# Kernel optimization log

Hardware: AMD Instinct MI355X
Metric: run time of the kernel (lower is better)

The kernel has to match this reference:

```python
import jax, jax.numpy as jnp
import numpy as np

B, H, S, DH = 2, 16, 2048, 64
MASK_FILL = -10000.0


def setup_inputs() -> dict:
    key = jax.random.key(0)
    kq, kk, kv = jax.random.split(key, 3)
    q = jax.random.normal(kq, (B, H, S, DH), dtype=jnp.float32)
    k = jax.random.normal(kk, (B, H, S, DH), dtype=jnp.float32)
    v = jax.random.normal(kv, (B, H, S, DH), dtype=jnp.float32)
    # causal mask: True where attention is disallowed (upper triangle)
    mask = jnp.triu(jnp.ones((S, S), dtype=jnp.bool_), k=1)
    return {"q": q, "k": k, "v": v, "mask": mask}


def reference(q, k, v, mask):
    scale = 1.0 / jnp.sqrt(jnp.asarray(k.shape[-1], dtype=q.dtype))
    # scores: [B, H, S_q, S_k]
    scores = jnp.einsum("bhqd,bhkd->bhqk", q, k) * scale
    # additive mask: masked_fill on a zeros [S_k, S_v] matrix -> -10000 where mask
    attn_bias = jnp.where(mask, jnp.asarray(MASK_FILL, dtype=k.dtype),
                          jnp.asarray(0.0, dtype=k.dtype))
    scores = scores + attn_bias  # broadcast over batch/heads
    attn = jax.nn.softmax(scores, axis=-1)
    # dropout_rate = 0.0 -> identity
    return jnp.einsum("bhqk,bhkd->bhqd", attn, v)
```

## Files before the change

kernel.cpp:

```cpp
#include <hip/hip_runtime.h>


#define S_LEN  2048
#define DHDIM  64
#define NHEADS 32
#define LDP    72
#define M2     23.083120654223414f
#define QSCALE 0.18033688011117658f

typedef __attribute__((ext_vector_type(8))) short bf16x8;
typedef __attribute__((ext_vector_type(4))) float f32x4;

__device__ __constant__ unsigned char T_QT[48] = {
    31,31,30,15, 30,29,29,28,14, 28,27,27,26,13, 26,25,25,24,12,
    24,23,23,22,11, 22,21,21,20,10, 20,19,19,18,9, 18,17,17,16,8,
    16,7, 6,5,4,3,2,1,0};
__device__ __constant__ unsigned char T_K0[48] = {
    0,16,0,0, 16,0,15,0,0, 15,0,14,0,0, 14,0,13,0,0,
    13,0,12,0,0, 12,0,11,0,0, 11,0,10,0,0, 10,0,9,0,0,
    9,0, 0,0,0,0,0,0,0};
__device__ __constant__ unsigned char T_K1[48] = {
    16,32,16,16, 31,15,30,15,15, 29,14,28,14,14, 27,13,26,13,13,
    25,12,24,12,12, 23,11,22,11,11, 21,10,20,10,10, 19,9,18,9,9,
    17,8, 7,6,5,4,3,2,1};

__device__ __forceinline__ float fast_exp2(float x) {
#if __has_builtin(__builtin_amdgcn_exp2f)
    return __builtin_amdgcn_exp2f(x);
#else
    return exp2f(x);
#endif
}
__device__ __forceinline__ unsigned short f2bf(float f) {
    unsigned u = __float_as_uint(f);
    return (unsigned short)((u + 0x7fffu + ((u >> 16) & 1u)) >> 16);
}
__device__ __forceinline__ void ld8(const float* p, float* f) {
    float4 a = *(const float4*)p, b = *(const float4*)(p + 4);
    f[0]=a.x; f[1]=a.y; f[2]=a.z; f[3]=a.w; f[4]=b.x; f[5]=b.y; f[6]=b.z; f[7]=b.w;
}
__device__ __forceinline__ uint4 pack8(const float* f, float scale) {
    union { uint4 v; unsigned short s[8]; } w;
    #pragma unroll
    for (int j = 0; j < 8; j++) w.s[j] = f2bf(f[j] * scale);
    return w.v;
}
__device__ __forceinline__ unsigned packhi(float a, float b) {
#if __has_builtin(__builtin_amdgcn_perm)
    return __builtin_amdgcn_perm(__float_as_uint(b), __float_as_uint(a), 0x07060302u);
#else
    return (__float_as_uint(a) >> 16) | (__float_as_uint(b) & 0xffff0000u);
#endif
}

__global__ __launch_bounds__(256) void prep(
    const float* __restrict__ Qf, const float* __restrict__ Kf,
    const float* __restrict__ Vf, unsigned short* __restrict__ qb,
    unsigned short* __restrict__ kb, unsigned short* __restrict__ vtb)
{
    const int st = blockIdx.x, bh = blockIdx.y;
    __shared__ unsigned lt32[64][LDP / 2];
    const float* vp = Vf + ((size_t)bh * S_LEN + st * 64) * DHDIM;
    {
        const int c = threadIdx.x;
        const int sp = c >> 3;
        const int d0 = (c & 7) * 8;
        float fa[8], fb[8];
        ld8(vp + (2 * sp) * DHDIM + d0, fa);
        ld8(vp + (2 * sp + 1) * DHDIM + d0, fb);
        #pragma unroll
        for (int j = 0; j < 8; j++) {
            int d = d0 + j;
            int colw = (sp & 3) | ((((sp >> 2) ^ (d >> 3)) & 7) << 2);
            lt32[d][colw] = (unsigned)f2bf(fa[j]) | ((unsigned)f2bf(fb[j]) << 16);
        }
    }
    size_t off = ((size_t)(bh * 32 + st) * 4096) + (size_t)threadIdx.x * 16;
    float f[8];
    ld8(Qf + off, f);     *(uint4*)(qb + off)     = pack8(f, QSCALE);
    ld8(Qf + off + 8, f); *(uint4*)(qb + off + 8) = pack8(f, QSCALE);
    ld8(Kf + off, f);     *(uint4*)(kb + off)     = pack8(f, 1.0f);
    ld8(Kf + off + 8, f); *(uint4*)(kb + off + 8) = pack8(f, 1.0f);
    __syncthreads();
    unsigned short* op = vtb + (size_t)bh * DHDIM * S_LEN + st * 64;
    for (int c = threadIdx.x; c < 512; c += 256) {
        int d = c >> 3, q = c & 7;
        int colw = ((q ^ (d >> 3)) & 7) << 2;
        *(uint4*)(op + (size_t)d * S_LEN + q * 8) = *(const uint4*)&lt32[d][colw & ~3 ? colw : colw];
    }
}

__global__ __launch_bounds__(256) void fattn_splitk(
    const unsigned short* __restrict__ Qp, const unsigned short* __restrict__ Kp,
    const unsigned short* __restrict__ Vp,
    float* __restrict__ pO, float* __restrict__ pL, float* __restrict__ O)
{
    __shared__ unsigned short smem[192 * LDP];
    unsigned short (*ks)[LDP]  = (unsigned short(*)[LDP])smem;
    unsigned short (*vts)[LDP] = (unsigned short(*)[LDP])(smem + 64 * LDP);
    unsigned short (*qs)[LDP]  = (unsigned short(*)[LDP])(smem + 128 * LDP);
    unsigned short (*pst)[LDP] = qs;

    const int bh   = blockIdx.x;
    const int rank = blockIdx.y;
    const int qt   = T_QT[rank];
    const int k0   = T_K0[rank];
    const int k1   = T_K1[rank];
    const bool whole = (k1 - k0 == qt + 1);

    const int tid = threadIdx.x;
    const int wave = tid >> 6, lane = tid & 63;
    const int quad = lane >> 4, l16 = lane & 15;

    {
        const unsigned short* src = Qp + ((size_t)bh * S_LEN + qt * 64) * DHDIM;
        for (int c = tid; c < 512; c += 256) {
            int row = c >> 3, c8 = (c & 7) * 8;
            *(uint4*)&qs[row][c8] = *(const uint4*)(src + row * DHDIM + c8);
        }
    }
    __syncthreads();

    const int prow = wave * 16 + l16;
    const bf16x8 bq0 = *(const bf16x8*)&qs[prow][quad * 8];
    const bf16x8 bq1 = *(const bf16x8*)&qs[prow][32 + quad * 8];

    bf16x8 ones;
    #pragma unroll
    for (int j = 0; j < 8; j++) ones[j] = (short)0x3F80;

    f32x4 of[4];
    f32x4 of_l = (f32x4){0.f, 0.f, 0.f, 0.f};
    #pragma unroll
    for (int n = 0; n < 4; n++) of[n] = (f32x4){0.f, 0.f, 0.f, 0.f};

    const unsigned short* Kbh = Kp + (size_t)bh * S_LEN * DHDIM;
    const unsigned short* Vbh = Vp + (size_t)bh * DHDIM * S_LEN;
    const int sr = tid >> 3, sc = (tid & 7) * 8;
    uint4 kr0, kr1, vr0, vr1;
    {
        const unsigned short* ksrc = Kbh + (size_t)k0 * 64 * DHDIM;
        const unsigned short* vsrc = Vbh + k0 * 64;
        kr0 = *(const uint4*)(ksrc + sr * DHDIM + sc);
        kr1 = *(const uint4*)(ksrc + (sr + 32) * DHDIM + sc);
        vr0 = *(const uint4*)(vsrc + (size_t)sr * S_LEN + sc);
        vr1 = *(const uint4*)(vsrc + (size_t)(sr + 32) * S_LEN + sc);
    }

    for (int kt = k0; kt < k1; kt++) {
        __syncthreads();

        *(uint4*)&ks[sr][sc]       = kr0;
        *(uint4*)&ks[sr + 32][sc]  = kr1;
        *(uint4*)&vts[sr][sc]      = vr0;
        *(uint4*)&vts[sr + 32][sc] = vr1;

        if (kt + 1 < k1) {
            const unsigned short* ksrc = Kbh + (size_t)(kt + 1) * 64 * DHDIM;
            const unsigned short* vsrc = Vbh + (kt + 1) * 64;
            kr0 = *(const uint4*)(ksrc + sr * DHDIM + sc);
            kr1 = *(const uint4*)(ksrc + (sr + 32) * DHDIM + sc);
            vr0 = *(const uint4*)(vsrc + (size_t)sr * S_LEN + sc);
            vr1 = *(const uint4*)(vsrc + (size_t)(sr + 32) * S_LEN + sc);
        }
        __syncthreads();

        f32x4 sf[4];
        #pragma unroll
        for (int n = 0; n < 4; n++) {
            bf16x8 ak0 = *(const bf16x8*)&ks[n * 16 + l16][quad * 8];
            bf16x8 ak1 = *(const bf16x8*)&ks[n * 16 + l16][32 + quad * 8];
            sf[n] = (f32x4){-M2, -M2, -M2, -M2};
            sf[n] = __builtin_amdgcn_mfma_f32_16x16x32_bf16(ak0, bq0, sf[n], 0, 0, 0);
            sf[n] = __builtin_amdgcn_mfma_f32_16x16x32_bf16(ak1, bq1, sf[n], 0, 0, 0);
        }

        const bool diag = (kt == qt);
        #pragma unroll
        for (int n = 0; n < 4; n++) {
            float p[4];
            #pragma unroll
            for (int r = 0; r < 4; r++) {
                p[r] = fast_exp2(sf[n][r]);
                if (diag && (n * 16 + quad * 4 + r > prow)) p[r] = 0.f;
            }
            uint2 dw;
            dw.x = packhi(p[0], p[1]);
            dw.y = packhi(p[2], p[3]);
            *(uint2*)&pst[prow][n * 16 + quad * 4] = dw;
        }
        asm volatile("s_waitcnt lgkmcnt(0)" ::: "memory");

        bf16x8 bp0 = *(const bf16x8*)&pst[prow][quad * 8];
        bf16x8 bp1 = *(const bf16x8*)&pst[prow][32 + quad * 8];
        of_l = __builtin_amdgcn_mfma_f32_16x16x32_bf16(ones, bp0, of_l, 0, 0, 0);
        of_l = __builtin_amdgcn_mfma_f32_16x16x32_bf16(ones, bp1, of_l, 0, 0, 0);
        #pragma unroll
        for (int n = 0; n < 4; n++) {
            bf16x8 av0 = *(const bf16x8*)&vts[n * 16 + l16][quad * 8];
            bf16x8 av1 = *(const bf16x8*)&vts[n * 16 + l16][32 + quad * 8];
            of[n] = __builtin_amdgcn_mfma_f32_16x16x32_bf16(av0, bp0, of[n], 0, 0, 0);
            of[n] = __builtin_amdgcn_mfma_f32_16x16x32_bf16(av1, bp1, of[n], 0, 0, 0);
        }
    }

    if (whole) {
        const float inv = 1.f / of_l[0];
        float* op = O + ((size_t)bh * S_LEN + qt * 64 + prow) * DHDIM;
        #pragma unroll
        for (int n = 0; n < 4; n++)
            *(float4*)(op + n * 16 + quad * 4) = make_float4(
                of[n][0] * inv, of[n][1] * inv, of[n][2] * inv, of[n][3] * inv);
    } else {
        const int slot = ((bh * 16 + (qt - 16)) << 1) | (k0 != 0 ? 1 : 0);
        if (quad == 0) pL[slot * 64 + prow] = of_l[0];
        float* op = pO + (size_t)slot * 4096 + prow * 64;
        #pragma unroll
        for (int n = 0; n < 4; n++)
            *(float4*)(op + n * 16 + quad * 4) =
                make_float4(of[n][0], of[n][1], of[n][2], of[n][3]);
    }
}

__global__ __launch_bounds__(256) void combine(
    const float* __restrict__ pO, const float* __restrict__ pL,
    float* __restrict__ O)
{
    const int qt = 16 + blockIdx.x, bh = blockIdx.y;
    const int sa = ((bh * 16 + (qt - 16)) << 1), sb = sa | 1;
    const float* A = pO + (size_t)sa * 4096;
    const float* B = pO + (size_t)sb * 4096;
    float* out = O + ((size_t)bh * S_LEN + qt * 64) * DHDIM;
    #pragma unroll
    for (int k = 0; k < 4; k++) {
        int c = threadIdx.x + k * 256;
        int row = c >> 4;
        float inv = 1.f / (pL[sa * 64 + row] + pL[sb * 64 + row]);
        float4 a = *(const float4*)(A + c * 4);
        float4 b = *(const float4*)(B + c * 4);
        *(float4*)(out + c * 4) = make_float4(
            (a.x + b.x) * inv, (a.y + b.y) * inv,
            (a.z + b.z) * inv, (a.w + b.w) * inv);
    }
}

template <bool PRE>
__global__ __launch_bounds__(256) void fattn_kernel(
    const void* __restrict__ Qp, const void* __restrict__ Kp,
    const void* __restrict__ Vp, float* __restrict__ O)
{
    __shared__ unsigned short smem[192 * LDP];
    unsigned short (*ks)[LDP]  = (unsigned short(*)[LDP])smem;
    unsigned short (*vts)[LDP] = (unsigned short(*)[LDP])(smem + 64 * LDP);
    unsigned short (*qs)[LDP]  = (unsigned short(*)[LDP])(smem + 128 * LDP);
    unsigned short (*pst)[LDP] = qs;

    const int id = blockIdx.y * 32 + blockIdx.x;
    const int g  = id >> 8;
    const int r8 = id & 255;
    const int bh = r8 >> 3;
    const int s8 = r8 & 7;
    const int qt = (g == 0) ? 31 - 2 * s8 : (g == 1) ? 2 * s8
                 : (g == 2) ? 30 - 2 * s8 : 2 * s8 + 1;

    const int tid = threadIdx.x;
    const int wave = tid >> 6, lane = tid & 63;
    const int quad = lane >> 4, l16 = lane & 15;

    if constexpr (PRE) {
        const unsigned short* src = (const unsigned short*)Qp
            + ((size_t)bh * S_LEN + qt * 64) * DHDIM;
        for (int c = tid; c < 512; c += 256) {
            int row = c >> 3, c8 = (c & 7) * 8;
            *(uint4*)&qs[row][c8] = *(const uint4*)(src + row * DHDIM + c8);
        }
    } else {
        const float* src = (const float*)Qp + ((size_t)bh * S_LEN + qt * 64) * DHDIM;
        for (int c = tid; c < 512; c += 256) {
            int row = c >> 3, c8 = (c & 7) * 8;
            float f[8]; ld8(src + row * DHDIM + c8, f);
            *(uint4*)&qs[row][c8] = pack8(f, QSCALE);
        }
    }
    __syncthreads();

    const int prow = wave * 16 + l16;
    const bf16x8 bq0 = *(const bf16x8*)&qs[prow][quad * 8];
    const bf16x8 bq1 = *(const bf16x8*)&qs[prow][32 + quad * 8];

    float l_p = 0.f;
    f32x4 of[4];
    #pragma unroll
    for (int n = 0; n < 4; n++) of[n] = (f32x4){0.f, 0.f, 0.f, 0.f};

    for (int kt = 0; kt <= qt; kt++) {
        __syncthreads();
        if constexpr (PRE) {
            const unsigned short* ksrc = (const unsigned short*)Kp
                + ((size_t)bh * S_LEN + kt * 64) * DHDIM;
            const unsigned short* vsrc = (const unsigned short*)Vp
                + (size_t)bh * DHDIM * S_LEN + kt * 64;
            for (int c = tid; c < 512; c += 256) {
                int row = c >> 3, c8 = (c & 7) * 8;
                *(uint4*)&ks[row][c8]  = *(const uint4*)(ksrc + row * DHDIM + c8);
                *(uint4*)&vts[row][c8] = *(const uint4*)(vsrc + (size_t)row * S_LEN + c8);
            }
        } else {
            const float* ksrc = (const float*)Kp + ((size_t)bh * S_LEN + kt * 64) * DHDIM;
            const float* vsrc = (const float*)Vp + ((size_t)bh * S_LEN + kt * 64) * DHDIM;
            for (int c = tid; c < 512; c += 256) {
                int row = c >> 3, c8 = (c & 7) * 8;
                float f[8];
                ld8(ksrc + row * DHDIM + c8, f);
                *(uint4*)&ks[row][c8] = pack8(f, 1.0f);
                ld8(vsrc + row * DHDIM + c8, f);
                #pragma unroll
                for (int j = 0; j < 8; j++) vts[c8 + j][row] = f2bf(f[j]);
            }
        }
        __syncthreads();

        f32x4 sf[4];
        #pragma unroll
        for (int n = 0; n < 4; n++) {
            bf16x8 ak0 = *(const bf16x8*)&ks[n * 16 + l16][quad * 8];
            bf16x8 ak1 = *(const bf16x8*)&ks[n * 16 + l16][32 + quad * 8];
            sf[n] = (f32x4){-M2, -M2, -M2, -M2};
            sf[n] = __builtin_amdgcn_mfma_f32_16x16x32_bf16(ak0, bq0, sf[n], 0, 0, 0);
            sf[n] = __builtin_amdgcn_mfma_f32_16x16x32_bf16(ak1, bq1, sf[n], 0, 0, 0);
        }

        const bool diag = (kt == qt);
        #pragma unroll
        for (int n = 0; n < 4; n++) {
            float p[4];
            #pragma unroll
            for (int r = 0; r < 4; r++) {
                p[r] = fast_exp2(sf[n][r]);
                if (diag && (n * 16 + quad * 4 + r > prow)) p[r] = 0.f;
                l_p += p[r];
            }
            uint2 dw;
            dw.x = packhi(p[0], p[1]);
            dw.y = packhi(p[2], p[3]);
            *(uint2*)&pst[prow][n * 16 + quad * 4] = dw;
        }
        asm volatile("s_waitcnt lgkmcnt(0)" ::: "memory");

        bf16x8 bp0 = *(const bf16x8*)&pst[prow][quad * 8];
        bf16x8 bp1 = *(const bf16x8*)&pst[prow][32 + quad * 8];
        #pragma unroll
        for (int n = 0; n < 4; n++) {
            bf16x8 av0 = *(const bf16x8*)&vts[n * 16 + l16][quad * 8];
            bf16x8 av1 = *(const bf16x8*)&vts[n * 16 + l16][32 + quad * 8];
            of[n] = __builtin_amdgcn_mfma_f32_16x16x32_bf16(av0, bp0, of[n], 0, 0, 0);
            of[n] = __builtin_amdgcn_mfma_f32_16x16x32_bf16(av1, bp1, of[n], 0, 0, 0);
        }
    }

    l_p += __shfl_xor(l_p, 16);
    l_p += __shfl_xor(l_p, 32);
    const float inv = 1.f / l_p;
    float* op = O + ((size_t)bh * S_LEN + qt * 64 + prow) * DHDIM;
    #pragma unroll
    for (int n = 0; n < 4; n++)
        *(float4*)(op + n * 16 + quad * 4) = make_float4(
            of[n][0] * inv, of[n][1] * inv, of[n][2] * inv, of[n][3] * inv);
}

extern "C" void kernel_launch(void* const* d_in, const int* in_sizes, int n_in,
                              void* d_out, int out_size, void* d_ws, size_t ws_size,
                              hipStream_t stream) {
    const float* Q = (const float*)d_in[0];
    const float* K = (const float*)d_in[1];
    const float* V = (const float*)d_in[2];
    float* O = (float*)d_out;
    const size_t N = (size_t)NHEADS * S_LEN * DHDIM;
    const size_t prepB  = 3 * N * sizeof(unsigned short);
    const size_t partB  = (size_t)1024 * (4096 + 64) * sizeof(float);

    if (d_ws && ws_size >= prepB + partB) {
        unsigned short* qb  = (unsigned short*)d_ws;
        unsigned short* kb  = qb + N;
        unsigned short* vtb = kb + N;
        float* pO = (float*)((char*)d_ws + prepB);
        float* pL = pO + (size_t)1024 * 4096;
        prep<<<dim3(S_LEN / 64, NHEADS), 256, 0, stream>>>(Q, K, V, qb, kb, vtb);
        fattn_splitk<<<dim3(32, 48), 256, 0, stream>>>(qb, kb, vtb, pO, pL, O);
        combine<<<dim3(16, 32), 256, 0, stream>>>(pO, pL, O);
    } else if (d_ws && ws_size >= prepB) {
        unsigned short* qb  = (unsigned short*)d_ws;
        unsigned short* kb  = qb + N;
        unsigned short* vtb = kb + N;
        prep<<<dim3(S_LEN / 64, NHEADS), 256, 0, stream>>>(Q, K, V, qb, kb, vtb);
        fattn_kernel<true><<<dim3(32, 32), 256, 0, stream>>>(qb, kb, vtb, O);
    } else {
        fattn_kernel<false><<<dim3(32, 32), 256, 0, stream>>>(Q, K, V, O);
    }
}
```

Baseline: 140.7 us.

## Split key tile across eight waves with double-buffered K/V and reduction

The split-K attention kernel moves to 512 threads: each wave owns a 16-key slice and 32 query rows, so P stays in registers (zero-padded K=16 MFMA inputs) instead of round-tripping through shared memory. K/V tiles are double-buffered in LDS, which leaves one barrier per iteration, and the per-slice partial outputs are summed through shared memory in a tree at the end. This trades half-empty MFMAs and an extra end-of-kernel reduction with several barriers for more waves per tile and fewer LDS round trips.

```diff
diff --git a/kernel.cpp b/kernel.cpp
--- a/kernel.cpp
+++ b/kernel.cpp
@@ -51,6 +51,11 @@
 #else
     return (__float_as_uint(a) >> 16) | (__float_as_uint(b) & 0xffff0000u);
 #endif
+}
+__device__ __forceinline__ bf16x8 pad4(unsigned lo, unsigned hi) {
+    union { unsigned u[4]; bf16x8 v; } w;
+    w.u[0] = lo; w.u[1] = hi; w.u[2] = 0u; w.u[3] = 0u;
+    return w.v;
 }
 
 __global__ __launch_bounds__(256) void prep(
@@ -86,20 +91,21 @@
     for (int c = threadIdx.x; c < 512; c += 256) {
         int d = c >> 3, q = c & 7;
         int colw = ((q ^ (d >> 3)) & 7) << 2;
-        *(uint4*)(op + (size_t)d * S_LEN + q * 8) = *(const uint4*)&lt32[d][colw & ~3 ? colw : colw];
-    }
-}
-
-__global__ __launch_bounds__(256) void fattn_splitk(
+        *(uint4*)(op + (size_t)d * S_LEN + q * 8) = *(const uint4*)&lt32[d][colw];
+    }
+}
+
+__global__ __launch_bounds__(512, 4) void fattn_splitk(
     const unsigned short* __restrict__ Qp, const unsigned short* __restrict__ Kp,
     const unsigned short* __restrict__ Vp,
     float* __restrict__ pO, float* __restrict__ pL, float* __restrict__ O)
 {
-    __shared__ unsigned short smem[192 * LDP];
-    unsigned short (*ks)[LDP]  = (unsigned short(*)[LDP])smem;
-    unsigned short (*vts)[LDP] = (unsigned short(*)[LDP])(smem + 64 * LDP);
-    unsigned short (*qs)[LDP]  = (unsigned short(*)[LDP])(smem + 128 * LDP);
-    unsigned short (*pst)[LDP] = qs;
+    __shared__ unsigned short smem[320 * LDP];
+    unsigned short (*ksA)[LDP] = (unsigned short(*)[LDP])smem;
+    unsigned short (*ksB)[LDP] = (unsigned short(*)[LDP])(smem + 64 * LDP);
+    unsigned short (*vtA)[LDP] = (unsigned short(*)[LDP])(smem + 128 * LDP);
+    unsigned short (*vtB)[LDP] = (unsigned short(*)[LDP])(smem + 192 * LDP);
+    unsigned short (*qs)[LDP]  = (unsigned short(*)[LDP])(smem + 256 * LDP);
 
     const int bh   = blockIdx.x;
     const int rank = blockIdx.y;
@@ -108,117 +114,194 @@
     const int k1   = T_K1[rank];
     const bool whole = (k1 - k0 == qt + 1);
 
-    const int tid = threadIdx.x;
+    const int tid  = threadIdx.x;
     const int wave = tid >> 6, lane = tid & 63;
     const int quad = lane >> 4, l16 = lane & 15;
+    const int kslice = wave & 3, qhalf = wave >> 2;
 
     {
         const unsigned short* src = Qp + ((size_t)bh * S_LEN + qt * 64) * DHDIM;
-        for (int c = tid; c < 512; c += 256) {
-            int row = c >> 3, c8 = (c & 7) * 8;
-            *(uint4*)&qs[row][c8] = *(const uint4*)(src + row * DHDIM + c8);
-        }
+        int row = tid >> 3, c8 = (tid & 7) * 8;
+        *(uint4*)&qs[row][c8] = *(const uint4*)(src + row * DHDIM + c8);
     }
     __syncthreads();
-
-    const int prow = wave * 16 + l16;
-    const bf16x8 bq0 = *(const bf16x8*)&qs[prow][quad * 8];
-    const bf16x8 bq1 = *(const bf16x8*)&qs[prow][32 + quad * 8];
-
-    bf16x8 ones;
-    #pragma unroll
-    for (int j = 0; j < 8; j++) ones[j] = (short)0x3F80;
-
-    f32x4 of[4];
-    f32x4 of_l = (f32x4){0.f, 0.f, 0.f, 0.f};
-    #pragma unroll
-    for (int n = 0; n < 4; n++) of[n] = (f32x4){0.f, 0.f, 0.f, 0.f};
+    const bf16x8 bq00 = *(const bf16x8*)&qs[qhalf * 32 + l16][quad * 8];
+    const bf16x8 bq01 = *(const bf16x8*)&qs[qhalf * 32 + l16][32 + quad * 8];
+    const bf16x8 bq10 = *(const bf16x8*)&qs[qhalf * 32 + 16 + l16][quad * 8];
+    const bf16x8 bq11 = *(const bf16x8*)&qs[qhalf * 32 + 16 + l16][32 + quad * 8];
+
+    bf16x8 ones8;
+    #pragma unroll
+    for (int j = 0; j < 8; j++) ones8[j] = (j < 4) ? (short)0x3F80 : (short)0;
+
+    f32x4 of[4][2];
+    #pragma unroll
+    for (int dg = 0; dg < 4; dg++) {
+        of[dg][0] = (f32x4){0.f, 0.f, 0.f, 0.f};
+        of[dg][1] = (f32x4){0.f, 0.f, 0.f, 0.f};
+    }
+    f32x4 ofl0 = (f32x4){0.f, 0.f, 0.f, 0.f};
+    f32x4 ofl1 = (f32x4){0.f, 0.f, 0.f, 0.f};
 
     const unsigned short* Kbh = Kp + (size_t)bh * S_LEN * DHDIM;
     const unsigned short* Vbh = Vp + (size_t)bh * DHDIM * S_LEN;
     const int sr = tid >> 3, sc = (tid & 7) * 8;
-    uint4 kr0, kr1, vr0, vr1;
+    uint4 kr, vr;
+    kr = *(const uint4*)(Kbh + ((size_t)k0 * 64 + sr) * DHDIM + sc);
+    vr = *(const uint4*)(Vbh + (size_t)sr * S_LEN + k0 * 64 + sc);
     {
-        const unsigned short* ksrc = Kbh + (size_t)k0 * 64 * DHDIM;
-        const unsigned short* vsrc = Vbh + k0 * 64;
-        kr0 = *(const uint4*)(ksrc + sr * DHDIM + sc);
-        kr1 = *(const uint4*)(ksrc + (sr + 32) * DHDIM + sc);
-        vr0 = *(const uint4*)(vsrc + (size_t)sr * S_LEN + sc);
-        vr1 = *(const uint4*)(vsrc + (size_t)(sr + 32) * S_LEN + sc);
+        unsigned short (*ks)[LDP] = (k0 & 1) ? ksB : ksA;
+        unsigned short (*vt)[LDP] = (k0 & 1) ? vtB : vtA;
+        *(uint4*)&ks[sr][sc] = kr;
+        *(uint4*)&vt[sr][sc] = vr;
+    }
+    if (k0 + 1 < k1) {
+        kr = *(const uint4*)(Kbh + ((size_t)(k0 + 1) * 64 + sr) * DHDIM + sc);
+        vr = *(const uint4*)(Vbh + (size_t)sr * S_LEN + (k0 + 1) * 64 + sc);
     }
 
     for (int kt = k0; kt < k1; kt++) {
         __syncthreads();
 
-        *(uint4*)&ks[sr][sc]       = kr0;
-        *(uint4*)&ks[sr + 32][sc]  = kr1;
-        *(uint4*)&vts[sr][sc]      = vr0;
-        *(uint4*)&vts[sr + 32][sc] = vr1;
-
         if (kt + 1 < k1) {
-            const unsigned short* ksrc = Kbh + (size_t)(kt + 1) * 64 * DHDIM;
-            const unsigned short* vsrc = Vbh + (kt + 1) * 64;
-            kr0 = *(const uint4*)(ksrc + sr * DHDIM + sc);
-            kr1 = *(const uint4*)(ksrc + (sr + 32) * DHDIM + sc);
-            vr0 = *(const uint4*)(vsrc + (size_t)sr * S_LEN + sc);
-            vr1 = *(const uint4*)(vsrc + (size_t)(sr + 32) * S_LEN + sc);
-        }
-        __syncthreads();
-
-        f32x4 sf[4];
-        #pragma unroll
-        for (int n = 0; n < 4; n++) {
-            bf16x8 ak0 = *(const bf16x8*)&ks[n * 16 + l16][quad * 8];
-            bf16x8 ak1 = *(const bf16x8*)&ks[n * 16 + l16][32 + quad * 8];
-            sf[n] = (f32x4){-M2, -M2, -M2, -M2};
-            sf[n] = __builtin_amdgcn_mfma_f32_16x16x32_bf16(ak0, bq0, sf[n], 0, 0, 0);
-            sf[n] = __builtin_amdgcn_mfma_f32_16x16x32_bf16(ak1, bq1, sf[n], 0, 0, 0);
-        }
+            unsigned short (*ks)[LDP] = ((kt + 1) & 1) ? ksB : ksA;
+            unsigned short (*vt)[LDP] = ((kt + 1) & 1) ? vtB : vtA;
+            *(uint4*)&ks[sr][sc] = kr;
+            *(uint4*)&vt[sr][sc] = vr;
+            if (kt + 2 < k1) {
+                kr = *(const uint4*)(Kbh + ((size_t)(kt + 2) * 64 + sr) * DHDIM + sc);
+                vr = *(const uint4*)(Vbh + (size_t)sr * S_LEN + (kt + 2) * 64 + sc);
+            }
+        }
+        const unsigned short (*ksc)[LDP] = (kt & 1) ? ksB : ksA;
+        const unsigned short (*vtc)[LDP] = (kt & 1) ? vtB : vtA;
+
+        const bf16x8 ak0 = *(const bf16x8*)&ksc[kslice * 16 + l16][quad * 8];
+        const bf16x8 ak1 = *(const bf16x8*)&ksc[kslice * 16 + l16][32 + quad * 8];
+        f32x4 sf0 = (f32x4){-M2, -M2, -M2, -M2};
+        f32x4 sf1 = (f32x4){-M2, -M2, -M2, -M2};
+        sf0 = __builtin_amdgcn_mfma_f32_16x16x32_bf16(ak0, bq00, sf0, 0, 0, 0);
+        sf0 = __builtin_amdgcn_mfma_f32_16x16x32_bf16(ak1, bq01, sf0, 0, 0, 0);
+        sf1 = __builtin_amdgcn_mfma_f32_16x16x32_bf16(ak0, bq10, sf1, 0, 0, 0);
+        sf1 = __builtin_amdgcn_mfma_f32_16x16x32_bf16(ak1, bq11, sf1, 0, 0, 0);
 
         const bool diag = (kt == qt);
-        #pragma unroll
-        for (int n = 0; n < 4; n++) {
-            float p[4];
-            #pragma unroll
-            for (int r = 0; r < 4; r++) {
-                p[r] = fast_exp2(sf[n][r]);
-                if (diag && (n * 16 + quad * 4 + r > prow)) p[r] = 0.f;
-            }
-            uint2 dw;
-            dw.x = packhi(p[0], p[1]);
-            dw.y = packhi(p[2], p[3]);
-            *(uint2*)&pst[prow][n * 16 + quad * 4] = dw;
-        }
-        asm volatile("s_waitcnt lgkmcnt(0)" ::: "memory");
-
-        bf16x8 bp0 = *(const bf16x8*)&pst[prow][quad * 8];
-        bf16x8 bp1 = *(const bf16x8*)&pst[prow][32 + quad * 8];
-        of_l = __builtin_amdgcn_mfma_f32_16x16x32_bf16(ones, bp0, of_l, 0, 0, 0);
-        of_l = __builtin_amdgcn_mfma_f32_16x16x32_bf16(ones, bp1, of_l, 0, 0, 0);
-        #pragma unroll
-        for (int n = 0; n < 4; n++) {
-            bf16x8 av0 = *(const bf16x8*)&vts[n * 16 + l16][quad * 8];
-            bf16x8 av1 = *(const bf16x8*)&vts[n * 16 + l16][32 + quad * 8];
-            of[n] = __builtin_amdgcn_mfma_f32_16x16x32_bf16(av0, bp0, of[n], 0, 0, 0);
-            of[n] = __builtin_amdgcn_mfma_f32_16x16x32_bf16(av1, bp1, of[n], 0, 0, 0);
-        }
-    }
-
-    if (whole) {
-        const float inv = 1.f / of_l[0];
-        float* op = O + ((size_t)bh * S_LEN + qt * 64 + prow) * DHDIM;
-        #pragma unroll
-        for (int n = 0; n < 4; n++)
-            *(float4*)(op + n * 16 + quad * 4) = make_float4(
-                of[n][0] * inv, of[n][1] * inv, of[n][2] * inv, of[n][3] * inv);
-    } else {
-        const int slot = ((bh * 16 + (qt - 16)) << 1) | (k0 != 0 ? 1 : 0);
-        if (quad == 0) pL[slot * 64 + prow] = of_l[0];
-        float* op = pO + (size_t)slot * 4096 + prow * 64;
-        #pragma unroll
-        for (int n = 0; n < 4; n++)
-            *(float4*)(op + n * 16 + quad * 4) =
-                make_float4(of[n][0], of[n][1], of[n][2], of[n][3]);
+        float p0[4], p1[4];
+        #pragma unroll
+        for (int r = 0; r < 4; r++) {
+            p0[r] = fast_exp2(sf0[r]);
+            p1[r] = fast_exp2(sf1[r]);
+            if (diag) {
+                const int kloc = kslice * 16 + quad * 4 + r;
+                if (kloc > qhalf * 32 + l16)      p0[r] = 0.f;
+                if (kloc > qhalf * 32 + 16 + l16) p1[r] = 0.f;
+            }
+        }
+        const bf16x8 bp0 = pad4(packhi(p0[0], p0[1]), packhi(p0[2], p0[3]));
+        const bf16x8 bp1 = pad4(packhi(p1[0], p1[1]), packhi(p1[2], p1[3]));
+        ofl0 = __builtin_amdgcn_mfma_f32_16x16x32_bf16(ones8, bp0, ofl0, 0, 0, 0);
+        ofl1 = __builtin_amdgcn_mfma_f32_16x16x32_bf16(ones8, bp1, ofl1, 0, 0, 0);
+
+        #pragma unroll
+        for (int dg = 0; dg < 4; dg++) {
+            const unsigned* vp32 =
+                (const unsigned*)&vtc[dg * 16 + l16][kslice * 16 + quad * 4];
+            const bf16x8 av = pad4(vp32[0], vp32[1]);
+            of[dg][0] = __builtin_amdgcn_mfma_f32_16x16x32_bf16(av, bp0, of[dg][0], 0, 0, 0);
+            of[dg][1] = __builtin_amdgcn_mfma_f32_16x16x32_bf16(av, bp1, of[dg][1], 0, 0, 0);
+        }
+    }
+
+    __syncthreads();
+    float* fs = (float*)smem;
+    const int rb = lane * 18;
+    #pragma unroll
+    for (int pass = 0; pass < 2; pass++) {
+        const int d0 = pass * 2;
+        if (kslice >= 2) {
+            float* w = fs + (qhalf * 2 + (kslice - 2)) * (64 * 18) + rb;
+            #pragma unroll
+            for (int d = 0; d < 2; d++)
+                #pragma unroll
+                for (int n2 = 0; n2 < 2; n2++)
+                    #pragma unroll
+                    for (int r = 0; r < 4; r++)
+                        w[d * 8 + n2 * 4 + r] = of[d0 + d][n2][r];
+            if (pass) { w[16] = ofl0[0]; w[17] = ofl1[0]; }
+        }
+        __syncthreads();
+        if (kslice < 2) {
+            const float* rd = fs + (qhalf * 2 + kslice) * (64 * 18) + rb;
+            #pragma unroll
+            for (int d = 0; d < 2; d++)
+                #pragma unroll
+                for (int n2 = 0; n2 < 2; n2++)
+                    #pragma unroll
+                    for (int r = 0; r < 4; r++)
+                        of[d0 + d][n2][r] += rd[d * 8 + n2 * 4 + r];
+            if (pass) { ofl0[0] += rd[16]; ofl1[0] += rd[17]; }
+        }
+        __syncthreads();
+        if (kslice == 1) {
+            float* w = fs + qhalf * (64 * 18) + rb;
+            #pragma unroll
+            for (int d = 0; d < 2; d++)
+                #pragma unroll
+                for (int n2 = 0; n2 < 2; n2++)
+                    #pragma unroll
+                    for (int r = 0; r < 4; r++)
+                        w[d * 8 + n2 * 4 + r] = of[d0 + d][n2][r];
+            if (pass) { w[16] = ofl0[0]; w[17] = ofl1[0]; }
+        }
+        __syncthreads();
+        if (kslice == 0) {
+            const float* rd = fs + qhalf * (64 * 18) + rb;
+            #pragma unroll
+            for (int d = 0; d < 2; d++)
+                #pragma unroll
+                for (int n2 = 0; n2 < 2; n2++)
+                    #pragma unroll
+                    for (int r = 0; r < 4; r++)
+                        of[d0 + d][n2][r] += rd[d * 8 + n2 * 4 + r];
+            if (pass) { ofl0[0] += rd[16]; ofl1[0] += rd[17]; }
+        }
+        __syncthreads();
+    }
+
+    if (kslice == 0) {
+        const int q0 = qt * 64 + qhalf * 32 + l16;
+        const int q1 = q0 + 16;
+        if (whole) {
+            const float inv0 = 1.f / ofl0[0];
+            const float inv1 = 1.f / ofl1[0];
+            float* o0 = O + ((size_t)bh * S_LEN + q0) * DHDIM;
+            float* o1 = O + ((size_t)bh * S_LEN + q1) * DHDIM;
+            #pragma unroll
+            for (int dg = 0; dg < 4; dg++) {
+                *(float4*)(o0 + dg * 16 + quad * 4) = make_float4(
+                    of[dg][0][0] * inv0, of[dg][0][1] * inv0,
+                    of[dg][0][2] * inv0, of[dg][0][3] * inv0);
+                *(float4*)(o1 + dg * 16 + quad * 4) = make_float4(
+                    of[dg][1][0] * inv1, of[dg][1][1] * inv1,
+                    of[dg][1][2] * inv1, of[dg][1][3] * inv1);
+            }
+        } else {
+            const int slot = ((bh * 16 + (qt - 16)) << 1) | (k0 != 0 ? 1 : 0);
+            const int r0 = qhalf * 32 + l16, r1 = r0 + 16;
+            if (quad == 0) {
+                pL[slot * 64 + r0] = ofl0[0];
+                pL[slot * 64 + r1] = ofl1[0];
+            }
+            float* p0p = pO + (size_t)slot * 4096 + r0 * 64;
+            float* p1p = pO + (size_t)slot * 4096 + r1 * 64;
+            #pragma unroll
+            for (int dg = 0; dg < 4; dg++) {
+                *(float4*)(p0p + dg * 16 + quad * 4) = make_float4(
+                    of[dg][0][0], of[dg][0][1], of[dg][0][2], of[dg][0][3]);
+                *(float4*)(p1p + dg * 16 + quad * 4) = make_float4(
+                    of[dg][1][0], of[dg][1][1], of[dg][1][2], of[dg][1][3]);
+            }
+        }
     }
 }
 
@@ -386,7 +469,7 @@
         float* pO = (float*)((char*)d_ws + prepB);
         float* pL = pO + (size_t)1024 * 4096;
         prep<<<dim3(S_LEN / 64, NHEADS), 256, 0, stream>>>(Q, K, V, qb, kb, vtb);
-        fattn_splitk<<<dim3(32, 48), 256, 0, stream>>>(qb, kb, vtb, pO, pL, O);
+        fattn_splitk<<<dim3(32, 48), 512, 0, stream>>>(qb, kb, vtb, pO, pL, O);
         combine<<<dim3(16, 32), 256, 0, stream>>>(pO, pL, O);
     } else if (d_ws && ws_size >= prepB) {
         unsigned short* qb  = (unsigned short*)d_ws;
```

Result: slower. 143.7 us (+2.1%).

## Rebalance causal split-K schedule into finer chunks and prioritize MFMA waves

Applied to the files above, without the earlier changes.

Replaces the 48-entry split-K work table with a 63-entry packed table. Query tiles 11–31 are now split into two or three key-range chunks of roughly 11 tiles or fewer, with explicit partial-output slots. This gives finer load balancing across more blocks, and the combine kernel is generalized to merge two or three partials. It also raises wave priority around the MFMA sections with s_setprio. The cost is more partial-output traffic, more workspace, and a heavier combine pass.

```diff
diff --git a/kernel.cpp b/kernel.cpp
--- a/kernel.cpp
+++ b/kernel.cpp
@@ -7,22 +7,32 @@
 #define LDP    72
 #define M2     23.083120654223414f
 #define QSCALE 0.18033688011117658f
+#define NSLOT  52
 
 typedef __attribute__((ext_vector_type(8))) short bf16x8;
 typedef __attribute__((ext_vector_type(4))) float f32x4;
 
-__device__ __constant__ unsigned char T_QT[48] = {
-    31,31,30,15, 30,29,29,28,14, 28,27,27,26,13, 26,25,25,24,12,
-    24,23,23,22,11, 22,21,21,20,10, 20,19,19,18,9, 18,17,17,16,8,
-    16,7, 6,5,4,3,2,1,0};
-__device__ __constant__ unsigned char T_K0[48] = {
-    0,16,0,0, 16,0,15,0,0, 15,0,14,0,0, 14,0,13,0,0,
-    13,0,12,0,0, 12,0,11,0,0, 11,0,10,0,0, 10,0,9,0,0,
-    9,0, 0,0,0,0,0,0,0};
-__device__ __constant__ unsigned char T_K1[48] = {
-    16,32,16,16, 31,15,30,15,15, 29,14,28,14,14, 27,13,26,13,13,
-    25,12,24,12,12, 23,11,22,11,11, 21,10,20,10,10, 19,9,18,9,9,
-    17,8, 7,6,5,4,3,2,1};
+#define RT(qt,k0,k1,sl) ((unsigned)(qt)<<24 | (unsigned)(k0)<<16 | (unsigned)(k1)<<8 | (unsigned)(sl))
+__device__ __constant__ unsigned RTAB[63] = {
+    RT(31,0,11,49),  RT(31,11,22,50), RT(30,0,11,46),  RT(21,0,11,20),
+    RT(21,11,22,21), RT(20,0,11,18),  RT(10,0,11,255),
+    RT(31,22,32,51), RT(30,11,21,47), RT(30,21,31,48), RT(29,0,10,43),
+    RT(29,10,20,44), RT(29,20,30,45), RT(28,0,10,40),  RT(28,10,20,41),
+    RT(27,0,10,37),  RT(20,11,21,19), RT(19,0,10,16),  RT(19,10,20,17),
+    RT(18,0,10,14),  RT(9,0,10,255),
+    RT(28,20,29,42), RT(27,10,19,38), RT(27,19,28,39), RT(26,0,9,34),
+    RT(26,9,18,35),  RT(26,18,27,36), RT(25,0,9,31),   RT(25,9,18,32),
+    RT(24,0,9,28),   RT(18,10,19,15), RT(17,0,9,12),   RT(17,9,18,13),
+    RT(16,0,9,10),   RT(8,0,9,255),
+    RT(25,18,26,33), RT(24,9,17,29),  RT(24,17,25,30), RT(23,0,8,25),
+    RT(23,8,16,26),  RT(23,16,24,27), RT(22,0,8,22),   RT(22,8,16,23),
+    RT(16,9,17,11),  RT(15,0,8,8),    RT(15,8,16,9),   RT(14,0,8,6),
+    RT(7,0,8,255),
+    RT(22,16,23,24), RT(14,8,15,7),   RT(13,0,7,4),    RT(13,7,14,5),
+    RT(12,0,7,2),    RT(6,0,7,255),
+    RT(12,7,13,3),   RT(11,0,6,0),    RT(11,6,12,1),   RT(5,0,6,255),
+    RT(4,0,5,255),   RT(3,0,4,255),   RT(2,0,3,255),   RT(1,0,2,255),
+    RT(0,0,1,255)};
 
 __device__ __forceinline__ float fast_exp2(float x) {
 #if __has_builtin(__builtin_amdgcn_exp2f)
@@ -86,7 +96,7 @@
     for (int c = threadIdx.x; c < 512; c += 256) {
         int d = c >> 3, q = c & 7;
         int colw = ((q ^ (d >> 3)) & 7) << 2;
-        *(uint4*)(op + (size_t)d * S_LEN + q * 8) = *(const uint4*)&lt32[d][colw & ~3 ? colw : colw];
+        *(uint4*)(op + (size_t)d * S_LEN + q * 8) = *(const uint4*)&lt32[d][colw];
     }
 }
 
@@ -102,11 +112,12 @@
     unsigned short (*pst)[LDP] = qs;
 
     const int bh   = blockIdx.x;
-    const int rank = blockIdx.y;
-    const int qt   = T_QT[rank];
-    const int k0   = T_K0[rank];
-    const int k1   = T_K1[rank];
-    const bool whole = (k1 - k0 == qt + 1);
+    const unsigned e = RTAB[blockIdx.y];
+    const int qt   = e >> 24;
+    const int k0   = (e >> 16) & 255;
+    const int k1   = (e >> 8) & 255;
+    const int sl   = e & 255;
+    const bool whole = (sl == 255);
 
     const int tid = threadIdx.x;
     const int wave = tid >> 6, lane = tid & 63;
@@ -165,6 +176,7 @@
         }
         __syncthreads();
 
+        __builtin_amdgcn_s_setprio(1);
         f32x4 sf[4];
         #pragma unroll
         for (int n = 0; n < 4; n++) {
@@ -174,6 +186,7 @@
             sf[n] = __builtin_amdgcn_mfma_f32_16x16x32_bf16(ak0, bq0, sf[n], 0, 0, 0);
             sf[n] = __builtin_amdgcn_mfma_f32_16x16x32_bf16(ak1, bq1, sf[n], 0, 0, 0);
         }
+        __builtin_amdgcn_s_setprio(0);
 
         const bool diag = (kt == qt);
         #pragma unroll
@@ -191,6 +204,7 @@
         }
         asm volatile("s_waitcnt lgkmcnt(0)" ::: "memory");
 
+        __builtin_amdgcn_s_setprio(1);
         bf16x8 bp0 = *(const bf16x8*)&pst[prow][quad * 8];
         bf16x8 bp1 = *(const bf16x8*)&pst[prow][32 + quad * 8];
         of_l = __builtin_amdgcn_mfma_f32_16x16x32_bf16(ones, bp0, of_l, 0, 0, 0);
@@ -202,6 +216,7 @@
             of[n] = __builtin_amdgcn_mfma_f32_16x16x32_bf16(av0, bp0, of[n], 0, 0, 0);
             of[n] = __builtin_amdgcn_mfma_f32_16x16x32_bf16(av1, bp1, of[n], 0, 0, 0);
         }
+        __builtin_amdgcn_s_setprio(0);
     }
 
     if (whole) {
@@ -212,7 +227,7 @@
             *(float4*)(op + n * 16 + quad * 4) = make_float4(
                 of[n][0] * inv, of[n][1] * inv, of[n][2] * inv, of[n][3] * inv);
     } else {
-        const int slot = ((bh * 16 + (qt - 16)) << 1) | (k0 != 0 ? 1 : 0);
+        const int slot = bh * NSLOT + sl;
         if (quad == 0) pL[slot * 64 + prow] = of_l[0];
         float* op = pO + (size_t)slot * 4096 + prow * 64;
         #pragma unroll
@@ -226,21 +241,29 @@
     const float* __restrict__ pO, const float* __restrict__ pL,
     float* __restrict__ O)
 {
-    const int qt = 16 + blockIdx.x, bh = blockIdx.y;
-    const int sa = ((bh * 16 + (qt - 16)) << 1), sb = sa | 1;
-    const float* A = pO + (size_t)sa * 4096;
-    const float* B = pO + (size_t)sb * 4096;
+    const int qt = 11 + blockIdx.x, bh = blockIdx.y;
+    int base, cnt;
+    if (qt < 22) { base = (qt - 11) * 2;      cnt = 2; }
+    else         { base = 22 + 3 * (qt - 22); cnt = 3; }
+    const int sb = bh * NSLOT + base;
+    const float* A = pO + (size_t)sb * 4096;
     float* out = O + ((size_t)bh * S_LEN + qt * 64) * DHDIM;
     #pragma unroll
     for (int k = 0; k < 4; k++) {
         int c = threadIdx.x + k * 256;
         int row = c >> 4;
-        float inv = 1.f / (pL[sa * 64 + row] + pL[sb * 64 + row]);
+        float l = pL[sb * 64 + row] + pL[(sb + 1) * 64 + row];
         float4 a = *(const float4*)(A + c * 4);
-        float4 b = *(const float4*)(B + c * 4);
+        float4 b = *(const float4*)(A + 4096 + c * 4);
+        float4 s = make_float4(a.x + b.x, a.y + b.y, a.z + b.z, a.w + b.w);
+        if (cnt == 3) {
+            l += pL[(sb + 2) * 64 + row];
+            float4 d = *(const float4*)(A + 8192 + c * 4);
+            s = make_float4(s.x + d.x, s.y + d.y, s.z + d.z, s.w + d.w);
+        }
+        float inv = 1.f / l;
         *(float4*)(out + c * 4) = make_float4(
-            (a.x + b.x) * inv, (a.y + b.y) * inv,
-            (a.z + b.z) * inv, (a.w + b.w) * inv);
+            s.x * inv, s.y * inv, s.z * inv, s.w * inv);
     }
 }
 
@@ -377,17 +400,17 @@
     float* O = (float*)d_out;
     const size_t N = (size_t)NHEADS * S_LEN * DHDIM;
     const size_t prepB  = 3 * N * sizeof(unsigned short);
-    const size_t partB  = (size_t)1024 * (4096 + 64) * sizeof(float);
+    const size_t partB  = (size_t)NSLOT * 32 * (4096 + 64) * sizeof(float);
 
     if (d_ws && ws_size >= prepB + partB) {
         unsigned short* qb  = (unsigned short*)d_ws;
         unsigned short* kb  = qb + N;
         unsigned short* vtb = kb + N;
         float* pO = (float*)((char*)d_ws + prepB);
-        float* pL = pO + (size_t)1024 * 4096;
+        float* pL = pO + (size_t)NSLOT * 32 * 4096;
         prep<<<dim3(S_LEN / 64, NHEADS), 256, 0, stream>>>(Q, K, V, qb, kb, vtb);
-        fattn_splitk<<<dim3(32, 48), 256, 0, stream>>>(qb, kb, vtb, pO, pL, O);
-        combine<<<dim3(16, 32), 256, 0, stream>>>(pO, pL, O);
+        fattn_splitk<<<dim3(32, 63), 256, 0, stream>>>(qb, kb, vtb, pO, pL, O);
+        combine<<<dim3(21, 32), 256, 0, stream>>>(pO, pL, O);
     } else if (d_ws && ws_size >= prepB) {
         unsigned short* qb  = (unsigned short*)d_ws;
         unsigned short* kb  = qb + N;
```

Measured after the change: 141.0 us. Within noise of the previous version (+0.2%).
